# Kernel optimization log

Hardware: AMD Instinct MI355X
Metric: run time of the kernel (lower is better)

Reference implementation:

```python
import jax, jax.numpy as jnp
import numpy as np

B, Q, S, H, D = 4, 1024, 2048, 32, 128  # batch, new tokens, cache capacity, heads, head_dim
SCALE = 0.08838834764831845  # 1/sqrt(128)


def setup_inputs() -> dict:
    key = jax.random.key(0)
    ks = jax.random.split(key, 7)
    query_states = jax.random.normal(ks[0], (B, Q, H, D), jnp.float32)
    key_states = jax.random.normal(ks[1], (B, Q, H, D), jnp.float32)
    value_states = jax.random.normal(ks[2], (B, Q, H, D), jnp.float32)
    k_cache = jax.random.normal(ks[3], (B, S, H, D), jnp.float32)
    v_cache = jax.random.normal(ks[4], (B, S, H, D), jnp.float32)
    q_lens = jax.random.randint(ks[5], (B,), 1, Q + 1).astype(jnp.int32)      # ragged new lengths
    cache_lens = jax.random.randint(ks[6], (B,), 0, Q + 1).astype(jnp.int32)  # prior context lengths
    return dict(query_states=query_states, key_states=key_states, value_states=value_states,
                k_cache=k_cache, v_cache=v_cache, q_lens=q_lens, cache_lens=cache_lens)


def _update_cache(cache, new, cache_lens, q_lens):
    # Per-sequence append: write new[b, :q_len[b]] into cache[b, cache_len[b]:cache_len[b]+q_len[b]]
    def upd(c, n, clen, qlen):
        j = jnp.arange(Q)
        idx = jnp.clip(clen + j, 0, S - 1)               # [Q]
        valid = j < qlen                                  # [Q]
        vals = jnp.where(valid[:, None, None], n, c[idx])  # keep old value where padded
        return c.at[idx].set(vals)
    return jax.vmap(upd)(cache, new, cache_lens, q_lens)


def reference(query_states, key_states, value_states, k_cache, v_cache, q_lens, cache_lens):
    kc = _update_cache(k_cache, key_states, cache_lens, q_lens)   # [B,S,H,D]
    vc = _update_cache(v_cache, value_states, cache_lens, q_lens)

    scores = jnp.einsum('bqhd,bkhd->bhqk', query_states, kc) * SCALE  # [B,H,Q,S]

    qi = jnp.arange(Q)
    kj = jnp.arange(S)
    # query i may attend to cache pos j iff j < cache_len + min(i+1, q_len)  (causal + segment bound)
    limit = cache_lens[:, None] + jnp.minimum(qi[None, :] + 1, q_lens[:, None])  # [B,Q]
    mask = kj[None, None, :] < limit[:, :, None]                                  # [B,Q,S]
    scores = jnp.where(mask[:, None, :, :], scores, -jnp.inf)
    probs = jax.nn.softmax(scores, axis=-1)

    out = jnp.einsum('bhqk,bkhd->bqhd', probs, vc)  # [B,Q,H,D]
    q_valid = (qi[None, :] < q_lens[:, None])[:, :, None, None]
    return jnp.where(q_valid, out, jnp.zeros((), out.dtype))
```

## Files before the change

### kernel.cpp

```cpp
#include <hip/hip_runtime.h>


#define BB 4
#define QQ 1024
#define SS 2048
#define HH 32
#define DD 128
#define QT 64
#define KT 32
#define NTILES 64
#define TILE_ELEMS 4096
#define NITEMS 2048

typedef __attribute__((ext_vector_type(8))) short short8;
typedef __attribute__((ext_vector_type(4))) float f32x4;
typedef __attribute__((ext_vector_type(16))) float f32x16;
typedef __attribute__((ext_vector_type(4))) unsigned int u32x4;
typedef __attribute__((ext_vector_type(8))) unsigned short u16x8;

__device__ __forceinline__ unsigned short f2bf(float f) {
    unsigned int u = __builtin_bit_cast(unsigned int, f);
    u += 0x7FFFu + ((u >> 16) & 1u);
    return (unsigned short)(u >> 16);
}
__device__ __forceinline__ unsigned int cvtpk(float lo, float hi) {
    unsigned int r;
    asm("v_cvt_pk_bf16_f32 %0, %1, %2" : "=v"(r) : "v"(lo), "v"(hi));
    return r;
}

__global__ __launch_bounds__(256)
void prep(const float* __restrict__ ks, const float* __restrict__ vs,
          const float* __restrict__ kc_, const float* __restrict__ vc,
          const int* __restrict__ qlens, const int* __restrict__ clens,
          unsigned short* __restrict__ Kws, unsigned short* __restrict__ Vws)
{
    const int tile = blockIdx.x, h = blockIdx.y, b = blockIdx.z;
    const int qlen = qlens[b], clen = clens[b];
    if (tile * KT >= clen + qlen) return;
    const int tid = threadIdx.x;
    unsigned short* kout = Kws + (((size_t)b * HH + h) * NTILES + tile) * TILE_ELEMS;
    unsigned short* vout = Vws + (((size_t)b * HH + h) * NTILES + tile) * TILE_ELEMS;

    #pragma unroll
    for (int h2 = 0; h2 < 2; ++h2) {
        const int idx8 = h2 * 2048 + tid * 8;
        const int c = idx8 >> 9, l = (idx8 >> 3) & 63;
        int key = tile * KT + (l & 31);
        const float* src;
        if (key < clen) {
            src = kc_ + (((size_t)b * SS + key) * HH + h) * DD;
        } else {
            int i2 = key - clen; if (i2 > QQ - 1) i2 = QQ - 1;
            src = ks + (((size_t)b * QQ + i2) * HH + h) * DD;
        }
        const int d0 = c * 16 + ((l >> 5) << 3);
        f32x4 a0 = *(const f32x4*)&src[d0];
        f32x4 a1 = *(const f32x4*)&src[d0 + 4];
        u16x8 w;
        w[0] = f2bf(a0[0]); w[1] = f2bf(a0[1]); w[2] = f2bf(a0[2]); w[3] = f2bf(a0[3]);
        w[4] = f2bf(a1[0]); w[5] = f2bf(a1[1]); w[6] = f2bf(a1[2]); w[7] = f2bf(a1[3]);
        *(u16x8*)&kout[idx8] = w;
    }
    #pragma unroll
    for (int h2 = 0; h2 < 2; ++h2) {
        const int idx8 = h2 * 2048 + tid * 8;
        const int a = idx8 >> 9, l = (idx8 >> 3) & 63;
        const int dchunk = a >> 1, kcc = a & 1;
        const int d = dchunk * 32 + (l & 31);
        const int kb = tile * KT + kcc * 16 + ((l >> 5) << 3);
        u16x8 w;
        #pragma unroll
        for (int e = 0; e < 8; ++e) {
            int key = kb + e;
            const float* src;
            if (key < clen) {
                src = vc + (((size_t)b * SS + key) * HH + h) * DD;
            } else {
                int i2 = key - clen; if (i2 > QQ - 1) i2 = QQ - 1;
                src = vs + (((size_t)b * QQ + i2) * HH + h) * DD;
            }
            w[e] = f2bf(src[d]);
        }
        *(u16x8*)&vout[idx8] = w;
    }
}

__global__ __launch_bounds__(128, 2)
void segattn_persist(const float* __restrict__ qs, const int* __restrict__ qlens,
                     const int* __restrict__ clens,
                     const unsigned short* __restrict__ Kws,
                     const unsigned short* __restrict__ Vws,
                     float* __restrict__ out, int* __restrict__ counter)
{
    __shared__ int s_item;
    alignas(16) __shared__ unsigned short KVl[2][8192];

    const int tid = threadIdx.x, w = tid >> 6, lane = tid & 63;
    const int q31 = lane & 31, hi = lane >> 5;
    const bool hiL = (hi != 0);
    const float psc = 0.08838834764831845f * 1.4426950408889634f;
    const int sbase = w * 2048 + lane * 8;

    for (;;) {
        if (tid == 0) s_item = atomicAdd(counter, 1);
        __syncthreads();
        const int idx = s_item;
        __syncthreads();
        if (idx >= NITEMS) break;

        const int qt = 15 - (idx >> 7);
        const int b = idx & 3, h = (idx >> 2) & 31;
        const int qlen = qlens[b], clen = clens[b];
        const int q0 = qt * QT;

        if (q0 >= qlen) {
            f32x4 z = {0.f, 0.f, 0.f, 0.f};
            #pragma unroll
            for (int i2 = 0; i2 < 16; ++i2) {
                int f = tid + i2 * 128;
                int r = f >> 5, d4 = f & 31;
                *(f32x4*)&out[(((size_t)b * QQ + q0 + r) * HH + h) * DD + d4 * 4] = z;
            }
            continue;
        }

        const int q = q0 + w * 32 + q31;
        const float* qp = qs + (((size_t)b * QQ + q) * HH + h) * DD;
        short8 qf[8];
        #pragma unroll
        for (int c = 0; c < 8; ++c) {
            const int d0 = c * 16 + hi * 8;
            f32x4 a0 = *(const f32x4*)&qp[d0];
            f32x4 a1 = *(const f32x4*)&qp[d0 + 4];
            short8 t;
            t[0] = (short)f2bf(a0[0] * psc); t[1] = (short)f2bf(a0[1] * psc);
            t[2] = (short)f2bf(a0[2] * psc); t[3] = (short)f2bf(a0[3] * psc);
            t[4] = (short)f2bf(a1[0] * psc); t[5] = (short)f2bf(a1[1] * psc);
            t[6] = (short)f2bf(a1[2] * psc); t[7] = (short)f2bf(a1[3] * psc);
            qf[c] = t;
        }

        const int lim_l = (q < qlen) ? (clen + q + 1) : 0;
        const int wq0 = q0 + w * 32;
        const int lim_min = (wq0 + 31 < qlen) ? (clen + wq0 + 1) : 0;

        float m_ = -3e38f, l_ = 0.f;
        f32x16 o0 = {0}, o1 = {0}, o2 = {0}, o3 = {0};

        const int kmax = clen + min(q0 + QT, qlen);
        const int nt = (kmax + KT - 1) / KT;
        const unsigned short* Kb = Kws + ((size_t)(b * HH + h)) * NTILES * TILE_ELEMS;
        const unsigned short* Vb = Vws + ((size_t)(b * HH + h)) * NTILES * TILE_ELEMS;

        {
            #pragma unroll
            for (int j = 0; j < 4; ++j) {
                u32x4 ak = *(const u32x4*)&Kb[sbase + j * 512];
                u32x4 av = *(const u32x4*)&Vb[sbase + j * 512];
                *(u32x4*)&KVl[0][sbase + j * 512]        = ak;
                *(u32x4*)&KVl[0][4096 + sbase + j * 512] = av;
            }
            asm volatile("s_waitcnt lgkmcnt(0)" ::: "memory");
            __builtin_amdgcn_s_barrier();
            __builtin_amdgcn_sched_barrier(0);
        }
        const int t1 = (nt > 1) ? 1 : 0;
        const unsigned short* kt1 = Kb + (size_t)t1 * TILE_ELEMS;
        const unsigned short* vt1 = Vb + (size_t)t1 * TILE_ELEMS;
        u32x4 sk0 = *(const u32x4*)&kt1[sbase];
        u32x4 sk1 = *(const u32x4*)&kt1[sbase + 512];
        u32x4 sk2 = *(const u32x4*)&kt1[sbase + 1024];
        u32x4 sk3 = *(const u32x4*)&kt1[sbase + 1536];
        u32x4 sv0 = *(const u32x4*)&vt1[sbase];
        u32x4 sv1 = *(const u32x4*)&vt1[sbase + 512];
        u32x4 sv2 = *(const u32x4*)&vt1[sbase + 1024];
        u32x4 sv3 = *(const u32x4*)&vt1[sbase + 1536];

        int cur = 0;
        for (int t = 0; t < nt; ++t) {
            const int nb = cur ^ 1;
            *(u32x4*)&KVl[nb][sbase]               = sk0;
            *(u32x4*)&KVl[nb][sbase + 512]         = sk1;
            *(u32x4*)&KVl[nb][sbase + 1024]        = sk2;
            *(u32x4*)&KVl[nb][sbase + 1536]        = sk3;
            *(u32x4*)&KVl[nb][4096 + sbase]        = sv0;
            *(u32x4*)&KVl[nb][4096 + sbase + 512]  = sv1;
            *(u32x4*)&KVl[nb][4096 + sbase + 1024] = sv2;
            *(u32x4*)&KVl[nb][4096 + sbase + 1536] = sv3;
            const int t2c = (t + 2 < nt) ? t + 2 : (nt - 1);
            const unsigned short* kt2 = Kb + (size_t)t2c * TILE_ELEMS;
            const unsigned short* vt2 = Vb + (size_t)t2c * TILE_ELEMS;
            sk0 = *(const u32x4*)&kt2[sbase];
            sk1 = *(const u32x4*)&kt2[sbase + 512];
            sk2 = *(const u32x4*)&kt2[sbase + 1024];
            sk3 = *(const u32x4*)&kt2[sbase + 1536];
            sv0 = *(const u32x4*)&vt2[sbase];
            sv1 = *(const u32x4*)&vt2[sbase + 512];
            sv2 = *(const u32x4*)&vt2[sbase + 1024];
            sv3 = *(const u32x4*)&vt2[sbase + 1536];
            asm volatile("s_waitcnt lgkmcnt(0)" ::: "memory");
            __builtin_amdgcn_s_barrier();
            __builtin_amdgcn_sched_barrier(0);

            const unsigned short* Kc = &KVl[cur][0];
            const int pbase = t * KT;
            f32x16 s = {0};
            #pragma unroll
            for (int c = 0; c < 8; ++c) {
                short8 kf = *(const short8*)&Kc[c * 512 + lane * 8];
                s = __builtin_amdgcn_mfma_f32_32x32x16_bf16(kf, qf[c], s, 0, 0, 0);
            }
            if (pbase + KT > lim_min) {
                #pragma unroll
                for (int r = 0; r < 16; ++r) {
                    const int kk = pbase + (r & 3) + ((r >> 2) << 3) + hi * 4;
                    if (kk >= lim_l) s[r] = -3e38f;
                }
            }
            float pm = fmaxf(fmaxf(fmaxf(fmaxf(s[0], s[1]), fmaxf(s[2], s[3])),
                                   fmaxf(fmaxf(s[4], s[5]), fmaxf(s[6], s[7]))),
                             fmaxf(fmaxf(fmaxf(s[8], s[9]), fmaxf(s[10], s[11])),
                                   fmaxf(fmaxf(s[12], s[13]), fmaxf(s[14], s[15]))));
            if (__any(pm > m_ + 8.0f)) {
                pm = fmaxf(pm, __shfl_xor(pm, 32));
                const float mn = fmaxf(m_, pm);
                const float alpha = __builtin_amdgcn_exp2f(m_ - mn);
                m_ = mn;
                l_ *= alpha;
                #pragma unroll
                for (int r = 0; r < 16; ++r) {
                    o0[r] *= alpha; o1[r] *= alpha; o2[r] *= alpha; o3[r] *= alpha;
                }
            }
            float p[16];
            #pragma unroll
            for (int r = 0; r < 16; ++r) p[r] = __builtin_amdgcn_exp2f(s[r] - m_);
            l_ += (((p[0]+p[1])+(p[2]+p[3])) + ((p[4]+p[5])+(p[6]+p[7])))
                + (((p[8]+p[9])+(p[10]+p[11])) + ((p[12]+p[13])+(p[14]+p[15])));

            const unsigned int w0 = cvtpk(p[0],  p[1]);
            const unsigned int w1 = cvtpk(p[2],  p[3]);
            const unsigned int w2 = cvtpk(p[4],  p[5]);
            const unsigned int w3 = cvtpk(p[6],  p[7]);
            const unsigned int w4 = cvtpk(p[8],  p[9]);
            const unsigned int w5 = cvtpk(p[10], p[11]);
            const unsigned int w6 = cvtpk(p[12], p[13]);
            const unsigned int w7 = cvtpk(p[14], p[15]);
            const unsigned int x0 = (unsigned int)__shfl_xor((int)w0, 32);
            const unsigned int x1 = (unsigned int)__shfl_xor((int)w1, 32);
            const unsigned int x2 = (unsigned int)__shfl_xor((int)w2, 32);
            const unsigned int x3 = (unsigned int)__shfl_xor((int)w3, 32);
            const unsigned int x4 = (unsigned int)__shfl_xor((int)w4, 32);
            const unsigned int x5 = (unsigned int)__shfl_xor((int)w5, 32);
            const unsigned int x6 = (unsigned int)__shfl_xor((int)w6, 32);
            const unsigned int x7 = (unsigned int)__shfl_xor((int)w7, 32);
            u32x4 pb0w, pb1w;
            pb0w[0] = hiL ? x2 : w0;  pb0w[1] = hiL ? x3 : w1;
            pb0w[2] = hiL ? w2 : x0;  pb0w[3] = hiL ? w3 : x1;
            pb1w[0] = hiL ? x6 : w4;  pb1w[1] = hiL ? x7 : w5;
            pb1w[2] = hiL ? w6 : x4;  pb1w[3] = hiL ? w7 : x5;
            const short8 pb0 = __builtin_bit_cast(short8, pb0w);
            const short8 pb1 = __builtin_bit_cast(short8, pb1w);

            {
                short8 va = *(const short8*)&Kc[4096 + 0 * 512 + lane * 8];
                short8 vb = *(const short8*)&Kc[4096 + 1 * 512 + lane * 8];
                o0 = __builtin_amdgcn_mfma_f32_32x32x16_bf16(va, pb0, o0, 0, 0, 0);
                o0 = __builtin_amdgcn_mfma_f32_32x32x16_bf16(vb, pb1, o0, 0, 0, 0);
            }
            {
                short8 va = *(const short8*)&Kc[4096 + 2 * 512 + lane * 8];
                short8 vb = *(const short8*)&Kc[4096 + 3 * 512 + lane * 8];
                o1 = __builtin_amdgcn_mfma_f32_32x32x16_bf16(va, pb0, o1, 0, 0, 0);
                o1 = __builtin_amdgcn_mfma_f32_32x32x16_bf16(vb, pb1, o1, 0, 0, 0);
            }
            {
                short8 va = *(const short8*)&Kc[4096 + 4 * 512 + lane * 8];
                short8 vb = *(const short8*)&Kc[4096 + 5 * 512 + lane * 8];
                o2 = __builtin_amdgcn_mfma_f32_32x32x16_bf16(va, pb0, o2, 0, 0, 0);
                o2 = __builtin_amdgcn_mfma_f32_32x32x16_bf16(vb, pb1, o2, 0, 0, 0);
            }
            {
                short8 va = *(const short8*)&Kc[4096 + 6 * 512 + lane * 8];
                short8 vb = *(const short8*)&Kc[4096 + 7 * 512 + lane * 8];
                o3 = __builtin_amdgcn_mfma_f32_32x32x16_bf16(va, pb0, o3, 0, 0, 0);
                o3 = __builtin_amdgcn_mfma_f32_32x32x16_bf16(vb, pb1, o3, 0, 0, 0);
            }

            asm volatile("s_waitcnt lgkmcnt(0)" ::: "memory");
            __builtin_amdgcn_s_barrier();
            __builtin_amdgcn_sched_barrier(0);
            cur = nb;
        }

        float lt = l_ + __shfl_xor(l_, 32);
        const bool val = (q < qlen);
        const float inv = val ? (1.0f / lt) : 0.f;
        float* op = out + (((size_t)b * QQ + q) * HH + h) * DD;
        #pragma unroll
        for (int rr = 0; rr < 4; ++rr) {
            f32x4 wv;
            const int d0 = rr * 8 + hi * 4;
            wv[0] = o0[rr*4+0]*inv; wv[1] = o0[rr*4+1]*inv;
            wv[2] = o0[rr*4+2]*inv; wv[3] = o0[rr*4+3]*inv;
            *(f32x4*)&op[d0] = wv;
            wv[0] = o1[rr*4+0]*inv; wv[1] = o1[rr*4+1]*inv;
            wv[2] = o1[rr*4+2]*inv; wv[3] = o1[rr*4+3]*inv;
            *(f32x4*)&op[32 + d0] = wv;
            wv[0] = o2[rr*4+0]*inv; wv[1] = o2[rr*4+1]*inv;
            wv[2] = o2[rr*4+2]*inv; wv[3] = o2[rr*4+3]*inv;
            *(f32x4*)&op[64 + d0] = wv;
            wv[0] = o3[rr*4+0]*inv; wv[1] = o3[rr*4+1]*inv;
            wv[2] = o3[rr*4+2]*inv; wv[3] = o3[rr*4+3]*inv;
            *(f32x4*)&op[96 + d0] = wv;
        }
    }
}

__global__ __launch_bounds__(256)
void segattn(const float* __restrict__ qs, const float* __restrict__ ks,
             const float* __restrict__ vs, const float* __restrict__ kc,
             const float* __restrict__ vc, const int* __restrict__ qlens,
             const int* __restrict__ clens, float* __restrict__ out)
{
    const int qt = blockIdx.x, h = blockIdx.y, b = blockIdx.z;
    const int tid = threadIdx.x, wave = tid >> 6, lane = tid & 63;
    const int g = lane >> 4, lc = lane & 15;
    const int qlen = qlens[b], clen = clens[b];
    const int q0 = qt * QT;
    if (q0 >= qlen) {
        f32x4 z = {0.f, 0.f, 0.f, 0.f};
        #pragma unroll
        for (int i2 = 0; i2 < 8; ++i2) {
            int f = tid + i2 * 256;
            int r = f >> 5, d4 = f & 31;
            *(f32x4*)&out[(((size_t)b * QQ + q0 + r) * HH + h) * DD + d4 * 4] = z;
        }
        return;
    }
    alignas(16) __shared__ unsigned short Kl[KT * DD];
    alignas(16) __shared__ unsigned short Vl[DD * 40];
    alignas(16) __shared__ unsigned short Pl[4][16][40];
    const float psc = 0.08838834764831845f * 1.4426950408889634f;
    const int qrow = q0 + wave * 16 + lc;
    const float* qp = qs + (((size_t)b * QQ + qrow) * HH + h) * DD;
    short8 qf[4];
    #pragma unroll
    for (int c = 0; c < 4; ++c) {
        f32x4 a0 = *(const f32x4*)&qp[c * 32 + g * 8];
        f32x4 a1 = *(const f32x4*)&qp[c * 32 + g * 8 + 4];
        short8 t;
        t[0] = (short)f2bf(a0[0] * psc); t[1] = (short)f2bf(a0[1] * psc);
        t[2] = (short)f2bf(a0[2] * psc); t[3] = (short)f2bf(a0[3] * psc);
        t[4] = (short)f2bf(a1[0] * psc); t[5] = (short)f2bf(a1[1] * psc);
        t[6] = (short)f2bf(a1[2] * psc); t[7] = (short)f2bf(a1[3] * psc);
        qf[c] = t;
    }
    f32x4 o[8];
    #pragma unroll
    for (int n = 0; n < 8; ++n) o[n] = (f32x4){0.f, 0.f, 0.f, 0.f};
    float m_[4] = {-3e38f, -3e38f, -3e38f, -3e38f};
    float l_[4] = {0.f, 0.f, 0.f, 0.f};
    int lim[4];
    #pragma unroll
    for (int qq = 0; qq < 4; ++qq) {
        int i = q0 + wave * 16 + g * 4 + qq;
        lim[qq] = (i < qlen) ? (clen + i + 1) : 0;
    }
    const int kmax = clen + min(q0 + QT, qlen);
    const int nt = (kmax + KT - 1) / KT;
    for (int t = 0; t < nt; ++t) {
        const int pbase = t * KT;
        __syncthreads();
        #pragma unroll
        for (int it = 0; it < 4; ++it) {
            int f = tid + it * 256;
            int key = f >> 5, d4 = f & 31;
            int p = pbase + key;
            const float *srck, *srcv;
            if (p < clen) {
                size_t off = (((size_t)b * SS + p) * HH + h) * DD + d4 * 4;
                srck = kc + off; srcv = vc + off;
            } else {
                int idx = p - clen; if (idx > QQ - 1) idx = QQ - 1;
                size_t off = (((size_t)b * QQ + idx) * HH + h) * DD + d4 * 4;
                srck = ks + off; srcv = vs + off;
            }
            f32x4 kv = *(const f32x4*)srck;
            f32x4 vv = *(const f32x4*)srcv;
            int ei = (key * DD + d4 * 4) ^ ((key & 7) << 3);
            typedef __attribute__((ext_vector_type(4))) unsigned short u16x4;
            u16x4 kb4 = {f2bf(kv[0]), f2bf(kv[1]), f2bf(kv[2]), f2bf(kv[3])};
            *(u16x4*)&Kl[ei] = kb4;
            int d0 = d4 * 4;
            Vl[(d0 + 0) * 40 + key] = f2bf(vv[0]);
            Vl[(d0 + 1) * 40 + key] = f2bf(vv[1]);
            Vl[(d0 + 2) * 40 + key] = f2bf(vv[2]);
            Vl[(d0 + 3) * 40 + key] = f2bf(vv[3]);
        }
        __syncthreads();
        f32x4 sc0 = {0.f, 0.f, 0.f, 0.f}, sc1 = {0.f, 0.f, 0.f, 0.f};
        #pragma unroll
        for (int c = 0; c < 4; ++c) {
            int i0 = (lc * DD + c * 32 + g * 8) ^ ((lc & 7) << 3);
            int i1 = ((16 + lc) * DD + c * 32 + g * 8) ^ (((16 + lc) & 7) << 3);
            short8 k0 = *(const short8*)&Kl[i0];
            short8 k1 = *(const short8*)&Kl[i1];
            sc0 = __builtin_amdgcn_mfma_f32_16x16x32_bf16(qf[c], k0, sc0, 0, 0, 0);
            sc1 = __builtin_amdgcn_mfma_f32_16x16x32_bf16(qf[c], k1, sc1, 0, 0, 0);
        }
        float pr0[4], pr1[4];
        #pragma unroll
        for (int qq = 0; qq < 4; ++qq) {
            float s0 = sc0[qq], s1 = sc1[qq];
            if (pbase + lc >= lim[qq])      s0 = -3e38f;
            if (pbase + 16 + lc >= lim[qq]) s1 = -3e38f;
            float pm = fmaxf(s0, s1);
            #pragma unroll
            for (int d2 = 1; d2 < 16; d2 <<= 1) pm = fmaxf(pm, __shfl_xor(pm, d2));
            float mn = fmaxf(m_[qq], pm);
            float alpha = exp2f(m_[qq] - mn);
            float p0 = exp2f(s0 - mn), p1 = exp2f(s1 - mn);
            float rs = p0 + p1;
            #pragma unroll
            for (int d2 = 1; d2 < 16; d2 <<= 1) rs += __shfl_xor(rs, d2);
            l_[qq] = l_[qq] * alpha + rs;
            m_[qq] = mn;
            pr0[qq] = p0; pr1[qq] = p1;
            #pragma unroll
            for (int n = 0; n < 8; ++n) o[n][qq] *= alpha;
        }
        #pragma unroll
        for (int qq = 0; qq < 4; ++qq) {
            Pl[wave][g * 4 + qq][lc]      = f2bf(pr0[qq]);
            Pl[wave][g * 4 + qq][16 + lc] = f2bf(pr1[qq]);
        }
        short8 pf = *(const short8*)&Pl[wave][lc][g * 8];
        #pragma unroll
        for (int n = 0; n < 8; ++n) {
            short8 vf = *(const short8*)&Vl[(n * 16 + lc) * 40 + g * 8];
            o[n] = __builtin_amdgcn_mfma_f32_16x16x32_bf16(pf, vf, o[n], 0, 0, 0);
        }
    }
    #pragma unroll
    for (int qq = 0; qq < 4; ++qq) {
        int i = q0 + wave * 16 + g * 4 + qq;
        bool val = (i < qlen);
        float inv = val ? (1.0f / l_[qq]) : 0.f;
        size_t ob = (((size_t)b * QQ + i) * HH + h) * DD + lc;
        #pragma unroll
        for (int n = 0; n < 8; ++n)
            out[ob + (size_t)n * 16] = val ? o[n][qq] * inv : 0.f;
    }
}

extern "C" void kernel_launch(void* const* d_in, const int* in_sizes, int n_in,
                              void* d_out, int out_size, void* d_ws, size_t ws_size,
                              hipStream_t stream) {
    const float* qs = (const float*)d_in[0];
    const float* ks = (const float*)d_in[1];
    const float* vs = (const float*)d_in[2];
    const float* kc = (const float*)d_in[3];
    const float* vc = (const float*)d_in[4];
    const int* ql = (const int*)d_in[5];
    const int* cl = (const int*)d_in[6];
    float* o = (float*)d_out;

    const size_t kv_elems = (size_t)BB * HH * NTILES * TILE_ELEMS;
    const size_t kv_bytes = kv_elems * 2 * sizeof(unsigned short);
    const size_t need = kv_bytes + 128;

    if (ws_size >= need) {
        unsigned short* Kws = (unsigned short*)d_ws;
        unsigned short* Vws = Kws + kv_elems;
        int* counter = (int*)((char*)d_ws + kv_bytes);
        hipMemsetAsync(counter, 0, sizeof(int), stream);
        dim3 pgrid(NTILES, HH, BB), pblk(256, 1, 1);
        hipLaunchKernelGGL(prep, pgrid, pblk, 0, stream, ks, vs, kc, vc, ql, cl, Kws, Vws);
        dim3 grid(1024, 1, 1), blk(128, 1, 1);
        hipLaunchKernelGGL(segattn_persist, grid, blk, 0, stream, qs, ql, cl, Kws, Vws, o, counter);
    } else {
        dim3 grid(QQ / QT, HH, BB), blk(256, 1, 1);
        hipLaunchKernelGGL(segattn, grid, blk, 0, stream, qs, ks, vs, kc, vc, ql, cl, o);
    }
}
```

Before: 169.6 us.

## Single-buffer LDS tiles and raise occupancy of persistent attention kernel

Replaces the double-buffered shared-memory K/V tile with a single 16KB buffer and reduces register prefetch depth from two tiles ahead to one. Launch bounds change from 2 to 4 blocks per SIMD-group target and the persistent grid doubles to 2048 blocks. The aim is more resident waves to hide latency through occupancy rather than in-block double buffering. In exchange, the global load for the next tile has less time to arrive before it is needed, and the tighter register budget may cause spills.

```diff
diff --git a/kernel.cpp b/kernel.cpp
--- a/kernel.cpp
+++ b/kernel.cpp
@@ -86,7 +86,7 @@
     }
 }
 
-__global__ __launch_bounds__(128, 2)
+__global__ __launch_bounds__(128, 4)
 void segattn_persist(const float* __restrict__ qs, const int* __restrict__ qlens,
                      const int* __restrict__ clens,
                      const unsigned short* __restrict__ Kws,
@@ -94,7 +94,7 @@
                      float* __restrict__ out, int* __restrict__ counter)
 {
     __shared__ int s_item;
-    alignas(16) __shared__ unsigned short KVl[2][8192];
+    alignas(16) __shared__ unsigned short KVl[8192];
 
     const int tid = threadIdx.x, w = tid >> 6, lane = tid & 63;
     const int q31 = lane & 31, hi = lane >> 5;
@@ -153,62 +153,44 @@
         const unsigned short* Kb = Kws + ((size_t)(b * HH + h)) * NTILES * TILE_ELEMS;
         const unsigned short* Vb = Vws + ((size_t)(b * HH + h)) * NTILES * TILE_ELEMS;
 
-        {
-            #pragma unroll
-            for (int j = 0; j < 4; ++j) {
-                u32x4 ak = *(const u32x4*)&Kb[sbase + j * 512];
-                u32x4 av = *(const u32x4*)&Vb[sbase + j * 512];
-                *(u32x4*)&KVl[0][sbase + j * 512]        = ak;
-                *(u32x4*)&KVl[0][4096 + sbase + j * 512] = av;
-            }
+        u32x4 sk0 = *(const u32x4*)&Kb[sbase];
+        u32x4 sk1 = *(const u32x4*)&Kb[sbase + 512];
+        u32x4 sk2 = *(const u32x4*)&Kb[sbase + 1024];
+        u32x4 sk3 = *(const u32x4*)&Kb[sbase + 1536];
+        u32x4 sv0 = *(const u32x4*)&Vb[sbase];
+        u32x4 sv1 = *(const u32x4*)&Vb[sbase + 512];
+        u32x4 sv2 = *(const u32x4*)&Vb[sbase + 1024];
+        u32x4 sv3 = *(const u32x4*)&Vb[sbase + 1536];
+
+        for (int t = 0; t < nt; ++t) {
+            *(u32x4*)&KVl[sbase]               = sk0;
+            *(u32x4*)&KVl[sbase + 512]         = sk1;
+            *(u32x4*)&KVl[sbase + 1024]        = sk2;
+            *(u32x4*)&KVl[sbase + 1536]        = sk3;
+            *(u32x4*)&KVl[4096 + sbase]        = sv0;
+            *(u32x4*)&KVl[4096 + sbase + 512]  = sv1;
+            *(u32x4*)&KVl[4096 + sbase + 1024] = sv2;
+            *(u32x4*)&KVl[4096 + sbase + 1536] = sv3;
+            const int tnx = (t + 1 < nt) ? t + 1 : (nt - 1);
+            const unsigned short* ktn = Kb + (size_t)tnx * TILE_ELEMS;
+            const unsigned short* vtn = Vb + (size_t)tnx * TILE_ELEMS;
+            sk0 = *(const u32x4*)&ktn[sbase];
+            sk1 = *(const u32x4*)&ktn[sbase + 512];
+            sk2 = *(const u32x4*)&ktn[sbase + 1024];
+            sk3 = *(const u32x4*)&ktn[sbase + 1536];
+            sv0 = *(const u32x4*)&vtn[sbase];
+            sv1 = *(const u32x4*)&vtn[sbase + 512];
+            sv2 = *(const u32x4*)&vtn[sbase + 1024];
+            sv3 = *(const u32x4*)&vtn[sbase + 1536];
             asm volatile("s_waitcnt lgkmcnt(0)" ::: "memory");
             __builtin_amdgcn_s_barrier();
             __builtin_amdgcn_sched_barrier(0);
-        }
-        const int t1 = (nt > 1) ? 1 : 0;
-        const unsigned short* kt1 = Kb + (size_t)t1 * TILE_ELEMS;
-        const unsigned short* vt1 = Vb + (size_t)t1 * TILE_ELEMS;
-        u32x4 sk0 = *(const u32x4*)&kt1[sbase];
-        u32x4 sk1 = *(const u32x4*)&kt1[sbase + 512];
-        u32x4 sk2 = *(const u32x4*)&kt1[sbase + 1024];
-        u32x4 sk3 = *(const u32x4*)&kt1[sbase + 1536];
-        u32x4 sv0 = *(const u32x4*)&vt1[sbase];
-        u32x4 sv1 = *(const u32x4*)&vt1[sbase + 512];
-        u32x4 sv2 = *(const u32x4*)&vt1[sbase + 1024];
-        u32x4 sv3 = *(const u32x4*)&vt1[sbase + 1536];
-
-        int cur = 0;
-        for (int t = 0; t < nt; ++t) {
-            const int nb = cur ^ 1;
-            *(u32x4*)&KVl[nb][sbase]               = sk0;
-            *(u32x4*)&KVl[nb][sbase + 512]         = sk1;
-            *(u32x4*)&KVl[nb][sbase + 1024]        = sk2;
-            *(u32x4*)&KVl[nb][sbase + 1536]        = sk3;
-            *(u32x4*)&KVl[nb][4096 + sbase]        = sv0;
-            *(u32x4*)&KVl[nb][4096 + sbase + 512]  = sv1;
-            *(u32x4*)&KVl[nb][4096 + sbase + 1024] = sv2;
-            *(u32x4*)&KVl[nb][4096 + sbase + 1536] = sv3;
-            const int t2c = (t + 2 < nt) ? t + 2 : (nt - 1);
-            const unsigned short* kt2 = Kb + (size_t)t2c * TILE_ELEMS;
-            const unsigned short* vt2 = Vb + (size_t)t2c * TILE_ELEMS;
-            sk0 = *(const u32x4*)&kt2[sbase];
-            sk1 = *(const u32x4*)&kt2[sbase + 512];
-            sk2 = *(const u32x4*)&kt2[sbase + 1024];
-            sk3 = *(const u32x4*)&kt2[sbase + 1536];
-            sv0 = *(const u32x4*)&vt2[sbase];
-            sv1 = *(const u32x4*)&vt2[sbase + 512];
-            sv2 = *(const u32x4*)&vt2[sbase + 1024];
-            sv3 = *(const u32x4*)&vt2[sbase + 1536];
-            asm volatile("s_waitcnt lgkmcnt(0)" ::: "memory");
-            __builtin_amdgcn_s_barrier();
-            __builtin_amdgcn_sched_barrier(0);
-
-            const unsigned short* Kc = &KVl[cur][0];
+
             const int pbase = t * KT;
             f32x16 s = {0};
             #pragma unroll
             for (int c = 0; c < 8; ++c) {
-                short8 kf = *(const short8*)&Kc[c * 512 + lane * 8];
+                short8 kf = *(const short8*)&KVl[c * 512 + lane * 8];
                 s = __builtin_amdgcn_mfma_f32_32x32x16_bf16(kf, qf[c], s, 0, 0, 0);
             }
             if (pbase + KT > lim_min) {
@@ -264,26 +246,26 @@
             const short8 pb1 = __builtin_bit_cast(short8, pb1w);
 
             {
-                short8 va = *(const short8*)&Kc[4096 + 0 * 512 + lane * 8];
-                short8 vb = *(const short8*)&Kc[4096 + 1 * 512 + lane * 8];
+                short8 va = *(const short8*)&KVl[4096 + 0 * 512 + lane * 8];
+                short8 vb = *(const short8*)&KVl[4096 + 1 * 512 + lane * 8];
                 o0 = __builtin_amdgcn_mfma_f32_32x32x16_bf16(va, pb0, o0, 0, 0, 0);
                 o0 = __builtin_amdgcn_mfma_f32_32x32x16_bf16(vb, pb1, o0, 0, 0, 0);
             }
             {
-                short8 va = *(const short8*)&Kc[4096 + 2 * 512 + lane * 8];
-                short8 vb = *(const short8*)&Kc[4096 + 3 * 512 + lane * 8];
+                short8 va = *(const short8*)&KVl[4096 + 2 * 512 + lane * 8];
+                short8 vb = *(const short8*)&KVl[4096 + 3 * 512 + lane * 8];
                 o1 = __builtin_amdgcn_mfma_f32_32x32x16_bf16(va, pb0, o1, 0, 0, 0);
                 o1 = __builtin_amdgcn_mfma_f32_32x32x16_bf16(vb, pb1, o1, 0, 0, 0);
             }
             {
-                short8 va = *(const short8*)&Kc[4096 + 4 * 512 + lane * 8];
-                short8 vb = *(const short8*)&Kc[4096 + 5 * 512 + lane * 8];
+                short8 va = *(const short8*)&KVl[4096 + 4 * 512 + lane * 8];
+                short8 vb = *(const short8*)&KVl[4096 + 5 * 512 + lane * 8];
                 o2 = __builtin_amdgcn_mfma_f32_32x32x16_bf16(va, pb0, o2, 0, 0, 0);
                 o2 = __builtin_amdgcn_mfma_f32_32x32x16_bf16(vb, pb1, o2, 0, 0, 0);
             }
             {
-                short8 va = *(const short8*)&Kc[4096 + 6 * 512 + lane * 8];
-                short8 vb = *(const short8*)&Kc[4096 + 7 * 512 + lane * 8];
+                short8 va = *(const short8*)&KVl[4096 + 6 * 512 + lane * 8];
+                short8 vb = *(const short8*)&KVl[4096 + 7 * 512 + lane * 8];
                 o3 = __builtin_amdgcn_mfma_f32_32x32x16_bf16(va, pb0, o3, 0, 0, 0);
                 o3 = __builtin_amdgcn_mfma_f32_32x32x16_bf16(vb, pb1, o3, 0, 0, 0);
             }
@@ -291,7 +273,6 @@
             asm volatile("s_waitcnt lgkmcnt(0)" ::: "memory");
             __builtin_amdgcn_s_barrier();
             __builtin_amdgcn_sched_barrier(0);
-            cur = nb;
         }
 
         float lt = l_ + __shfl_xor(l_, 32);
@@ -478,7 +459,7 @@
         hipMemsetAsync(counter, 0, sizeof(int), stream);
         dim3 pgrid(NTILES, HH, BB), pblk(256, 1, 1);
         hipLaunchKernelGGL(prep, pgrid, pblk, 0, stream, ks, vs, kc, vc, ql, cl, Kws, Vws);
-        dim3 grid(1024, 1, 1), blk(128, 1, 1);
+        dim3 grid(2048, 1, 1), blk(128, 1, 1);
         hipLaunchKernelGGL(segattn_persist, grid, blk, 0, stream, qs, ql, cl, Kws, Vws, o, counter);
     } else {
         dim3 grid(QQ / QT, HH, BB), blk(256, 1, 1);
```

After: 346.8 us. +104.5%, slower.

## Load KV tiles directly into LDS with global_load_lds and raise MFMA priority

Applied to the files above, without the earlier changes.

Replaces the register-staged double buffer (global load to VGPRs, then LDS store, prefetched two tiles ahead) with direct global-to-LDS async loads that prefetch the next tile into the alternate buffer. This drops the VGPR staging and the LDS write instructions, cutting register pressure and VALU/LDS traffic. The prefetch distance shrinks from two tiles to one, and waits switch to vmcnt at the end of each iteration. It also wraps the MFMA sections in s_setprio to favour matrix issue among co-resident waves.

```diff
diff --git a/kernel.cpp b/kernel.cpp
--- a/kernel.cpp
+++ b/kernel.cpp
@@ -27,6 +27,11 @@
     unsigned int r;
     asm("v_cvt_pk_bf16_f32 %0, %1, %2" : "=v"(r) : "v"(lo), "v"(hi));
     return r;
+}
+__device__ __forceinline__ void glds16(const unsigned short* g, unsigned short* l) {
+    __builtin_amdgcn_global_load_lds(
+        (const __attribute__((address_space(1))) unsigned int*)g,
+        (__attribute__((address_space(3))) unsigned int*)l, 16, 0, 0);
 }
 
 __global__ __launch_bounds__(256)
@@ -101,6 +106,7 @@
     const bool hiL = (hi != 0);
     const float psc = 0.08838834764831845f * 1.4426950408889634f;
     const int sbase = w * 2048 + lane * 8;
+    const int lbase = w * 2048;
 
     for (;;) {
         if (tid == 0) s_item = atomicAdd(counter, 1);
@@ -153,64 +159,37 @@
         const unsigned short* Kb = Kws + ((size_t)(b * HH + h)) * NTILES * TILE_ELEMS;
         const unsigned short* Vb = Vws + ((size_t)(b * HH + h)) * NTILES * TILE_ELEMS;
 
-        {
-            #pragma unroll
-            for (int j = 0; j < 4; ++j) {
-                u32x4 ak = *(const u32x4*)&Kb[sbase + j * 512];
-                u32x4 av = *(const u32x4*)&Vb[sbase + j * 512];
-                *(u32x4*)&KVl[0][sbase + j * 512]        = ak;
-                *(u32x4*)&KVl[0][4096 + sbase + j * 512] = av;
-            }
-            asm volatile("s_waitcnt lgkmcnt(0)" ::: "memory");
-            __builtin_amdgcn_s_barrier();
-            __builtin_amdgcn_sched_barrier(0);
-        }
-        const int t1 = (nt > 1) ? 1 : 0;
-        const unsigned short* kt1 = Kb + (size_t)t1 * TILE_ELEMS;
-        const unsigned short* vt1 = Vb + (size_t)t1 * TILE_ELEMS;
-        u32x4 sk0 = *(const u32x4*)&kt1[sbase];
-        u32x4 sk1 = *(const u32x4*)&kt1[sbase + 512];
-        u32x4 sk2 = *(const u32x4*)&kt1[sbase + 1024];
-        u32x4 sk3 = *(const u32x4*)&kt1[sbase + 1536];
-        u32x4 sv0 = *(const u32x4*)&vt1[sbase];
-        u32x4 sv1 = *(const u32x4*)&vt1[sbase + 512];
-        u32x4 sv2 = *(const u32x4*)&vt1[sbase + 1024];
-        u32x4 sv3 = *(const u32x4*)&vt1[sbase + 1536];
+        #pragma unroll
+        for (int j = 0; j < 4; ++j) {
+            glds16(&Kb[sbase + j * 512], &KVl[0][lbase + j * 512]);
+            glds16(&Vb[sbase + j * 512], &KVl[0][4096 + lbase + j * 512]);
+        }
+        asm volatile("s_waitcnt vmcnt(0)" ::: "memory");
+        __builtin_amdgcn_s_barrier();
+        __builtin_amdgcn_sched_barrier(0);
 
         int cur = 0;
         for (int t = 0; t < nt; ++t) {
             const int nb = cur ^ 1;
-            *(u32x4*)&KVl[nb][sbase]               = sk0;
-            *(u32x4*)&KVl[nb][sbase + 512]         = sk1;
-            *(u32x4*)&KVl[nb][sbase + 1024]        = sk2;
-            *(u32x4*)&KVl[nb][sbase + 1536]        = sk3;
-            *(u32x4*)&KVl[nb][4096 + sbase]        = sv0;
-            *(u32x4*)&KVl[nb][4096 + sbase + 512]  = sv1;
-            *(u32x4*)&KVl[nb][4096 + sbase + 1024] = sv2;
-            *(u32x4*)&KVl[nb][4096 + sbase + 1536] = sv3;
-            const int t2c = (t + 2 < nt) ? t + 2 : (nt - 1);
-            const unsigned short* kt2 = Kb + (size_t)t2c * TILE_ELEMS;
-            const unsigned short* vt2 = Vb + (size_t)t2c * TILE_ELEMS;
-            sk0 = *(const u32x4*)&kt2[sbase];
-            sk1 = *(const u32x4*)&kt2[sbase + 512];
-            sk2 = *(const u32x4*)&kt2[sbase + 1024];
-            sk3 = *(const u32x4*)&kt2[sbase + 1536];
-            sv0 = *(const u32x4*)&vt2[sbase];
-            sv1 = *(const u32x4*)&vt2[sbase + 512];
-            sv2 = *(const u32x4*)&vt2[sbase + 1024];
-            sv3 = *(const u32x4*)&vt2[sbase + 1536];
-            asm volatile("s_waitcnt lgkmcnt(0)" ::: "memory");
-            __builtin_amdgcn_s_barrier();
-            __builtin_amdgcn_sched_barrier(0);
+            const int tnx = (t + 1 < nt) ? t + 1 : (nt - 1);
+            const unsigned short* ktn = Kb + (size_t)tnx * TILE_ELEMS;
+            const unsigned short* vtn = Vb + (size_t)tnx * TILE_ELEMS;
+            #pragma unroll
+            for (int j = 0; j < 4; ++j) {
+                glds16(&ktn[sbase + j * 512], &KVl[nb][lbase + j * 512]);
+                glds16(&vtn[sbase + j * 512], &KVl[nb][4096 + lbase + j * 512]);
+            }
 
             const unsigned short* Kc = &KVl[cur][0];
             const int pbase = t * KT;
             f32x16 s = {0};
+            __builtin_amdgcn_s_setprio(1);
             #pragma unroll
             for (int c = 0; c < 8; ++c) {
                 short8 kf = *(const short8*)&Kc[c * 512 + lane * 8];
                 s = __builtin_amdgcn_mfma_f32_32x32x16_bf16(kf, qf[c], s, 0, 0, 0);
             }
+            __builtin_amdgcn_s_setprio(0);
             if (pbase + KT > lim_min) {
                 #pragma unroll
                 for (int r = 0; r < 16; ++r) {
@@ -263,6 +242,7 @@
             const short8 pb0 = __builtin_bit_cast(short8, pb0w);
             const short8 pb1 = __builtin_bit_cast(short8, pb1w);
 
+            __builtin_amdgcn_s_setprio(1);
             {
                 short8 va = *(const short8*)&Kc[4096 + 0 * 512 + lane * 8];
                 short8 vb = *(const short8*)&Kc[4096 + 1 * 512 + lane * 8];
@@ -287,8 +267,9 @@
                 o3 = __builtin_amdgcn_mfma_f32_32x32x16_bf16(va, pb0, o3, 0, 0, 0);
                 o3 = __builtin_amdgcn_mfma_f32_32x32x16_bf16(vb, pb1, o3, 0, 0, 0);
             }
-
-            asm volatile("s_waitcnt lgkmcnt(0)" ::: "memory");
+            __builtin_amdgcn_s_setprio(0);
+
+            asm volatile("s_waitcnt vmcnt(0)" ::: "memory");
             __builtin_amdgcn_s_barrier();
             __builtin_amdgcn_sched_barrier(0);
             cur = nb;
```

Result: slower. 173.2 us (+2.1%).
